# Kernel optimization log

Hardware: AMD Instinct MI355X
Metric: run time of the kernel (lower is better)

## Reference

```python
import jax, jax.numpy as jnp
import numpy as np

VX, VY = 0.2, 0.2
X_OFFSET = VX / 2 + 0.0      # pc_range[0] = 0
Y_OFFSET = VY / 2 + (-40.0)  # pc_range[1] = -40
BN_EPS = 1e-3
IN_CH, OUT_CH = 9, 64


def setup_inputs() -> dict:
    key = jax.random.key(0)
    k1, k2, k3, k4 = jax.random.split(key, 4)
    bs, V, P = 2, 12000, 100
    features = jax.random.normal(k1, (bs, V, P, 4), dtype=jnp.float32)
    num_points = jax.random.randint(k2, (bs, V), 0, 100, dtype=jnp.int32)
    coors = jax.random.randint(k3, (bs, V, 4), 0, 352, dtype=jnp.int32)
    W = jax.random.normal(k4, (IN_CH, OUT_CH), dtype=jnp.float32) * 0.1
    gamma = jnp.ones((OUT_CH,), dtype=jnp.float32)
    beta = jnp.zeros((OUT_CH,), dtype=jnp.float32)
    return {"features": features, "num_points": num_points, "coors": coors,
            "W": W, "gamma": gamma, "beta": beta}


def reference(features, num_points, coors, W, gamma, beta):
    bs, V, P, _ = features.shape
    dt = features.dtype
    npf = num_points.astype(dt)

    # cluster features: offset from per-pillar mean of xyz
    points_mean = features[..., :3].sum(axis=2, keepdims=True) / jnp.maximum(npf, 1.0)[:, :, None, None]
    f_cluster = features[..., :3] - points_mean

    # center features: offset from pillar center (coors[...,2] = x idx, coors[...,1] = y idx)
    coors_f = coors.astype(dt)
    fcx = features[..., 0] - (coors_f[:, :, 2][:, :, None] * VX + X_OFFSET)
    fcy = features[..., 1] - (coors_f[:, :, 1][:, :, None] * VY + Y_OFFSET)
    f_center = jnp.stack([fcx, fcy], axis=-1)

    feats = jnp.concatenate([features, f_cluster, f_center], axis=-1)  # [bs,V,P,9]

    # padding mask over points in each pillar
    mask = (num_points[:, :, None] > jnp.arange(P)).astype(dt)[..., None]
    feats = feats * mask

    # PFNLayer (last layer): Linear(no bias) -> BatchNorm1d(train-mode stats) -> ReLU -> max over points
    x = jnp.einsum('bvpi,io->bvpo', feats, W)  # [bs,V,P,64]
    mean = x.mean(axis=(0, 1, 2))
    var = x.var(axis=(0, 1, 2))  # biased variance, as torch BN uses for normalization
    x = (x - mean) * jax.lax.rsqrt(var + BN_EPS) * gamma + beta
    x = jax.nn.relu(x)
    return x.max(axis=2)  # [bs,V,64]
```

## Files before the change

### kernel.cpp

```cpp
#include <hip/hip_runtime.h>
#include <math.h>

#define NP 100
#define NPILLAR 24000
#define OUT_CH 64
#define NTOTAL 2400000.0
#define VXc 0.2f
#define VYc 0.2f
#define XOFF 0.1f
#define YOFF (-39.9f)
#define BN_EPS 1e-3
#define SB 1024

typedef __attribute__((ext_vector_type(8))) short bf16x8;
typedef __attribute__((ext_vector_type(16))) float f32x16;
typedef __attribute__((ext_vector_type(4))) unsigned int uint4v;

__device__ __forceinline__ unsigned int f2bf(float x) {
    unsigned int b = __builtin_bit_cast(unsigned int, x);
    b += 0x7FFFu + ((b >> 16) & 1u);
    return b >> 16;
}

__device__ __forceinline__ void build_f(const float4 p, float mx, float my, float mz,
                                        float cx, float cy, float* f) {
    f[0] = p.x; f[1] = p.y; f[2] = p.z; f[3] = p.w;
    f[4] = p.x - mx; f[5] = p.y - my; f[6] = p.z - mz;
    f[7] = p.x - cx; f[8] = p.y - cy;
}

__global__ __launch_bounds__(256) void pfn_stats(
    const float4* __restrict__ feat, const int* __restrict__ npts,
    const int* __restrict__ coors, float* __restrict__ part)
{
    const int tid = threadIdx.x;
    const int lane = tid & 63;
    const int wv = tid >> 6;
    const int gw = blockIdx.x * 4 + wv;
    const int nw = SB * 4;

    float s[54];
#pragma unroll
    for (int i = 0; i < 54; ++i) s[i] = 0.f;

    for (int pv = gw; pv < NPILLAR; pv += nw) {
        const float4* fp = feat + (size_t)pv * NP;
        float4 p0 = fp[lane];
        float4 p1 = (lane + 64 < NP) ? fp[lane + 64] : make_float4(0.f, 0.f, 0.f, 0.f);

        float sx = p0.x + p1.x, sy = p0.y + p1.y, sz = p0.z + p1.z;
#pragma unroll
        for (int off = 32; off; off >>= 1) {
            sx += __shfl_xor(sx, off);
            sy += __shfl_xor(sy, off);
            sz += __shfl_xor(sz, off);
        }
        int np_ = npts[pv];
        if (np_ > NP) np_ = NP;
        float inv = 1.f / fmaxf((float)np_, 1.f);
        float mx = sx * inv, my = sy * inv, mz = sz * inv;
        float cx = (float)coors[pv * 4 + 2] * VXc + XOFF;
        float cy = (float)coors[pv * 4 + 1] * VYc + YOFF;

        float f[9];
        if (lane < np_) {
            build_f(p0, mx, my, mz, cx, cy, f);
            int k = 9;
#pragma unroll
            for (int i = 0; i < 9; ++i) {
                s[i] += f[i];
#pragma unroll
                for (int j = i; j < 9; ++j) s[k++] = fmaf(f[i], f[j], s[k]);
            }
        }
        if (lane + 64 < np_) {
            build_f(p1, mx, my, mz, cx, cy, f);
            int k = 9;
#pragma unroll
            for (int i = 0; i < 9; ++i) {
                s[i] += f[i];
#pragma unroll
                for (int j = i; j < 9; ++j) s[k++] = fmaf(f[i], f[j], s[k]);
            }
        }
    }

#pragma unroll
    for (int i = 0; i < 54; ++i) {
#pragma unroll
        for (int off = 32; off; off >>= 1) s[i] += __shfl_xor(s[i], off);
    }

    __shared__ float red[4][54];
    if (lane == 0) {
#pragma unroll
        for (int i = 0; i < 54; ++i) red[wv][i] = s[i];
    }
    __syncthreads();
    if (tid < 64) {
        float v = 0.f;
        if (tid < 54)
            v = red[0][tid] + red[1][tid] + red[2][tid] + red[3][tid];
        part[blockIdx.x * 64 + tid] = v;
    }
}

__global__ __launch_bounds__(1024) void pfn_finalize(
    const float* __restrict__ part, const float* __restrict__ W,
    const float* __restrict__ gamma, const float* __restrict__ beta,
    float* __restrict__ scsh)
{
    __shared__ double red[16][64];
    __shared__ double dm[64];
    const int t = threadIdx.x;
    const int m = t & 63;
    const int chunk = t >> 6;

    double s = 0.0;
#pragma unroll 8
    for (int b = chunk * 64; b < chunk * 64 + 64; ++b)
        s += (double)part[b * 64 + m];
    red[chunk][m] = s;
    __syncthreads();
    if (t < 64) {
        double tot = 0.0;
#pragma unroll
        for (int c = 0; c < 16; ++c) tot += red[c][t];
        dm[t] = tot;
    }
    __syncthreads();
    if (t < 64) {
        double w[9];
#pragma unroll
        for (int i = 0; i < 9; ++i) w[i] = (double)W[i * OUT_CH + t];
        double mean = 0.0;
#pragma unroll
        for (int i = 0; i < 9; ++i) mean += dm[i] * w[i];
        mean /= NTOTAL;
        double ex2 = 0.0;
        int k = 9;
#pragma unroll
        for (int i = 0; i < 9; ++i) {
#pragma unroll
            for (int j = i; j < 9; ++j) {
                double c = dm[k++];
                ex2 += (i == j ? 1.0 : 2.0) * c * w[i] * w[j];
            }
        }
        ex2 /= NTOTAL;
        double var = ex2 - mean * mean;
        double scale = (double)gamma[t] / sqrt(var + BN_EPS);
        double shift = (double)beta[t] - mean * scale;
        scsh[t] = (float)scale;
        scsh[OUT_CH + t] = (float)shift;
    }
}

__global__ __launch_bounds__(256) void pfn_out(
    const float4* __restrict__ feat, const int* __restrict__ npts,
    const int* __restrict__ coors, const float* __restrict__ W,
    const float* __restrict__ scsh, float* __restrict__ out)
{
    const int tid = threadIdx.x;
    const int lane = tid & 63;
    const int wv = tid >> 6;
    const int pv = blockIdx.x * 4 + wv;

    const int col = lane & 31;
    const int kbase = (lane >> 5) * 8;
    bf16x8 bfr0, bfr1;
#pragma unroll
    for (int i = 0; i < 8; ++i) {
        int k = kbase + i;
        float w0 = (k < 9) ? W[k * OUT_CH + col] : 0.f;
        float w1 = (k < 9) ? W[k * OUT_CH + 32 + col] : 0.f;
        bfr0[i] = (short)f2bf(w0);
        bfr1[i] = (short)f2bf(w1);
    }

    const float4* fp = feat + (size_t)pv * NP;
    float4 p0 = fp[lane];
    float4 p1 = (lane + 64 < NP) ? fp[lane + 64] : make_float4(0.f, 0.f, 0.f, 0.f);

    float sx = p0.x + p1.x, sy = p0.y + p1.y, sz = p0.z + p1.z;
#pragma unroll
    for (int off = 32; off; off >>= 1) {
        sx += __shfl_xor(sx, off);
        sy += __shfl_xor(sy, off);
        sz += __shfl_xor(sz, off);
    }
    int np_ = npts[pv];
    if (np_ > NP) np_ = NP;
    float inv = 1.f / fmaxf((float)np_, 1.f);
    float mx = sx * inv, my = sy * inv, mz = sz * inv;
    float cx = (float)coors[pv * 4 + 2] * VXc + XOFF;
    float cy = (float)coors[pv * 4 + 1] * VYc + YOFF;

    unsigned int A[5], B[5];
    {
        float f[9];
        if (lane < np_) {
            build_f(p0, mx, my, mz, cx, cy, f);
            A[0] = f2bf(f[0]) | (f2bf(f[1]) << 16);
            A[1] = f2bf(f[2]) | (f2bf(f[3]) << 16);
            A[2] = f2bf(f[4]) | (f2bf(f[5]) << 16);
            A[3] = f2bf(f[6]) | (f2bf(f[7]) << 16);
            A[4] = f2bf(f[8]);
        } else {
#pragma unroll
            for (int i = 0; i < 5; ++i) A[i] = 0u;
        }
        if (lane + 64 < np_) {
            build_f(p1, mx, my, mz, cx, cy, f);
            B[0] = f2bf(f[0]) | (f2bf(f[1]) << 16);
            B[1] = f2bf(f[2]) | (f2bf(f[3]) << 16);
            B[2] = f2bf(f[4]) | (f2bf(f[5]) << 16);
            B[3] = f2bf(f[6]) | (f2bf(f[7]) << 16);
            B[4] = f2bf(f[8]);
        } else {
#pragma unroll
            for (int i = 0; i < 5; ++i) B[i] = 0u;
        }
    }

    f32x16 cz;
#pragma unroll
    for (int i = 0; i < 16; ++i) cz[i] = 0.f;

    float xmx0 = -INFINITY, xmx1 = -INFINITY;
    float xmn0 = INFINITY, xmn1 = INFINITY;
    const bool lo = (lane < 32);
    const int nmt = (np_ + 31) >> 5;

    for (int mt = 0; mt < nmt; ++mt) {
        const int src = ((mt & 1) << 5) + col;
        unsigned int w0, w1, w2, w3, w4;
        if (mt < 2) {
            w0 = __shfl((int)A[0], src); w1 = __shfl((int)A[1], src);
            w2 = __shfl((int)A[2], src); w3 = __shfl((int)A[3], src);
            w4 = __shfl((int)A[4], src);
        } else {
            w0 = __shfl((int)B[0], src); w1 = __shfl((int)B[1], src);
            w2 = __shfl((int)B[2], src); w3 = __shfl((int)B[3], src);
            w4 = __shfl((int)B[4], src);
        }
        uint4v av = {lo ? w0 : w4, lo ? w1 : 0u, lo ? w2 : 0u, lo ? w3 : 0u};
        bf16x8 afr = __builtin_bit_cast(bf16x8, av);

        f32x16 c0 = __builtin_amdgcn_mfma_f32_32x32x16_bf16(afr, bfr0, cz, 0, 0, 0);
        f32x16 c1 = __builtin_amdgcn_mfma_f32_32x32x16_bf16(afr, bfr1, cz, 0, 0, 0);
#pragma unroll
        for (int r = 0; r < 16; r += 2) {
            xmx0 = fmaxf(xmx0, fmaxf(c0[r], c0[r + 1]));
            xmn0 = fminf(xmn0, fminf(c0[r], c0[r + 1]));
            xmx1 = fmaxf(xmx1, fmaxf(c1[r], c1[r + 1]));
            xmn1 = fminf(xmn1, fminf(c1[r], c1[r + 1]));
        }
    }

    if (np_ < NP) {
        xmx0 = fmaxf(xmx0, 0.f); xmx1 = fmaxf(xmx1, 0.f);
        xmn0 = fminf(xmn0, 0.f); xmn1 = fminf(xmn1, 0.f);
    }

    xmx0 = fmaxf(xmx0, __shfl_xor(xmx0, 32));
    xmx1 = fmaxf(xmx1, __shfl_xor(xmx1, 32));
    xmn0 = fminf(xmn0, __shfl_xor(xmn0, 32));
    xmn1 = fminf(xmn1, __shfl_xor(xmn1, 32));

    float xmx = lo ? xmx0 : xmx1;
    float xmn = lo ? xmn0 : xmn1;
    float scale = scsh[lane];
    float shift = scsh[OUT_CH + lane];
    out[(size_t)pv * OUT_CH + lane] =
        fmaxf(fmaf(scale, (scale >= 0.f) ? xmx : xmn, shift), 0.f);
}

extern "C" void kernel_launch(void* const* d_in, const int* in_sizes, int n_in,
                              void* d_out, int out_size, void* d_ws, size_t ws_size,
                              hipStream_t stream) {
    const float4* feat = (const float4*)d_in[0];
    const int* npts    = (const int*)d_in[1];
    const int* coors   = (const int*)d_in[2];
    const float* W     = (const float*)d_in[3];
    const float* gamma = (const float*)d_in[4];
    const float* beta  = (const float*)d_in[5];

    float* part = (float*)d_ws;
    float* scsh = part + SB * 64;

    pfn_stats<<<SB, 256, 0, stream>>>(feat, npts, coors, part);
    pfn_finalize<<<1, 1024, 0, stream>>>(part, W, gamma, beta, scsh);
    pfn_out<<<NPILLAR / 4, 256, 0, stream>>>(feat, npts, coors, W, scsh,
                                             (float*)d_out);
}
```

Before: 53.53 us.

## Fuse stats and matmul into one pass over features, apply BN in second kernel

Merges the statistics pass and the MFMA projection/max pass so the 38 MB feature tensor is read once instead of twice. Per-pillar raw max and min of the projected values go to workspace, and a new apply kernel computes BN scale/shift from the partial moments and applies them elementwise. This drops one kernel launch and one full feature read, at the cost of writing and reading two 6 MB max/min buffers and redundantly recomputing the finalize reduction in every apply block. It also clamps max/min against zero unconditionally for every pillar.

```diff
diff --git a/kernel.cpp b/kernel.cpp
--- a/kernel.cpp
+++ b/kernel.cpp
@@ -10,7 +10,9 @@
 #define XOFF 0.1f
 #define YOFF (-39.9f)
 #define BN_EPS 1e-3
-#define SB 1024
+#define G1 1024
+#define NWAVE1 (G1 * 4)
+#define G2 256
 
 typedef __attribute__((ext_vector_type(8))) short bf16x8;
 typedef __attribute__((ext_vector_type(16))) float f32x16;
@@ -29,21 +31,48 @@
     f[7] = p.x - cx; f[8] = p.y - cy;
 }
 
-__global__ __launch_bounds__(256) void pfn_stats(
+__device__ __forceinline__ void moments(float* s, const float* f) {
+    int k = 9;
+#pragma unroll
+    for (int i = 0; i < 9; ++i) {
+        s[i] += f[i];
+#pragma unroll
+        for (int j = i; j < 9; ++j) { s[k] = fmaf(f[i], f[j], s[k]); ++k; }
+    }
+}
+
+__global__ __launch_bounds__(256, 3) void pfn_main(
     const float4* __restrict__ feat, const int* __restrict__ npts,
-    const int* __restrict__ coors, float* __restrict__ part)
+    const int* __restrict__ coors, const float* __restrict__ W,
+    float* __restrict__ xmax_ws, float* __restrict__ xmin_ws,
+    float* __restrict__ part)
 {
     const int tid = threadIdx.x;
     const int lane = tid & 63;
     const int wv = tid >> 6;
     const int gw = blockIdx.x * 4 + wv;
-    const int nw = SB * 4;
+
+    const int col = lane & 31;
+    const int kbase = (lane >> 5) * 8;
+    const bool lo = (lane < 32);
+    bf16x8 bfr0, bfr1;
+#pragma unroll
+    for (int i = 0; i < 8; ++i) {
+        int k = kbase + i;
+        float w0 = (k < 9) ? W[k * OUT_CH + col] : 0.f;
+        float w1 = (k < 9) ? W[k * OUT_CH + 32 + col] : 0.f;
+        bfr0[i] = (short)f2bf(w0);
+        bfr1[i] = (short)f2bf(w1);
+    }
+    f32x16 cz;
+#pragma unroll
+    for (int i = 0; i < 16; ++i) cz[i] = 0.f;
 
     float s[54];
 #pragma unroll
     for (int i = 0; i < 54; ++i) s[i] = 0.f;
 
-    for (int pv = gw; pv < NPILLAR; pv += nw) {
+    for (int pv = gw; pv < NPILLAR; pv += NWAVE1) {
         const float4* fp = feat + (size_t)pv * NP;
         float4 p0 = fp[lane];
         float4 p1 = (lane + 64 < NP) ? fp[lane + 64] : make_float4(0.f, 0.f, 0.f, 0.f);
@@ -62,27 +91,78 @@
         float cx = (float)coors[pv * 4 + 2] * VXc + XOFF;
         float cy = (float)coors[pv * 4 + 1] * VYc + YOFF;
 
-        float f[9];
-        if (lane < np_) {
-            build_f(p0, mx, my, mz, cx, cy, f);
-            int k = 9;
-#pragma unroll
-            for (int i = 0; i < 9; ++i) {
-                s[i] += f[i];
-#pragma unroll
-                for (int j = i; j < 9; ++j) s[k++] = fmaf(f[i], f[j], s[k]);
-            }
-        }
-        if (lane + 64 < np_) {
-            build_f(p1, mx, my, mz, cx, cy, f);
-            int k = 9;
-#pragma unroll
-            for (int i = 0; i < 9; ++i) {
-                s[i] += f[i];
-#pragma unroll
-                for (int j = i; j < 9; ++j) s[k++] = fmaf(f[i], f[j], s[k]);
-            }
-        }
+        unsigned int A[5], B[5];
+        {
+            float f[9];
+            if (lane < np_) {
+                build_f(p0, mx, my, mz, cx, cy, f);
+                moments(s, f);
+                A[0] = f2bf(f[0]) | (f2bf(f[1]) << 16);
+                A[1] = f2bf(f[2]) | (f2bf(f[3]) << 16);
+                A[2] = f2bf(f[4]) | (f2bf(f[5]) << 16);
+                A[3] = f2bf(f[6]) | (f2bf(f[7]) << 16);
+                A[4] = f2bf(f[8]);
+            } else {
+#pragma unroll
+                for (int i = 0; i < 5; ++i) A[i] = 0u;
+            }
+            if (lane + 64 < np_) {
+                build_f(p1, mx, my, mz, cx, cy, f);
+                moments(s, f);
+                B[0] = f2bf(f[0]) | (f2bf(f[1]) << 16);
+                B[1] = f2bf(f[2]) | (f2bf(f[3]) << 16);
+                B[2] = f2bf(f[4]) | (f2bf(f[5]) << 16);
+                B[3] = f2bf(f[6]) | (f2bf(f[7]) << 16);
+                B[4] = f2bf(f[8]);
+            } else {
+#pragma unroll
+                for (int i = 0; i < 5; ++i) B[i] = 0u;
+            }
+        }
+
+        float xmx0 = -INFINITY, xmx1 = -INFINITY;
+        float xmn0 = INFINITY, xmn1 = INFINITY;
+        const int nmt = (np_ + 31) >> 5;
+
+        for (int mt = 0; mt < nmt; ++mt) {
+            const int src = ((mt & 1) << 5) + col;
+            unsigned int w0, w1, w2, w3, w4;
+            if (mt < 2) {
+                w0 = __shfl((int)A[0], src); w1 = __shfl((int)A[1], src);
+                w2 = __shfl((int)A[2], src); w3 = __shfl((int)A[3], src);
+                w4 = __shfl((int)A[4], src);
+            } else {
+                w0 = __shfl((int)B[0], src); w1 = __shfl((int)B[1], src);
+                w2 = __shfl((int)B[2], src); w3 = __shfl((int)B[3], src);
+                w4 = __shfl((int)B[4], src);
+            }
+            uint4v av = {lo ? w0 : w4, lo ? w1 : 0u, lo ? w2 : 0u, lo ? w3 : 0u};
+            bf16x8 afr = __builtin_bit_cast(bf16x8, av);
+
+            f32x16 c0 = __builtin_amdgcn_mfma_f32_32x32x16_bf16(afr, bfr0, cz, 0, 0, 0);
+#pragma unroll
+            for (int r = 0; r < 16; r += 2) {
+                xmx0 = fmaxf(xmx0, fmaxf(c0[r], c0[r + 1]));
+                xmn0 = fminf(xmn0, fminf(c0[r], c0[r + 1]));
+            }
+            f32x16 c1 = __builtin_amdgcn_mfma_f32_32x32x16_bf16(afr, bfr1, cz, 0, 0, 0);
+#pragma unroll
+            for (int r = 0; r < 16; r += 2) {
+                xmx1 = fmaxf(xmx1, fmaxf(c1[r], c1[r + 1]));
+                xmn1 = fminf(xmn1, fminf(c1[r], c1[r + 1]));
+            }
+        }
+
+        xmx0 = fmaxf(xmx0, 0.f); xmx1 = fmaxf(xmx1, 0.f);
+        xmn0 = fminf(xmn0, 0.f); xmn1 = fminf(xmn1, 0.f);
+
+        xmx0 = fmaxf(xmx0, __shfl_xor(xmx0, 32));
+        xmx1 = fmaxf(xmx1, __shfl_xor(xmx1, 32));
+        xmn0 = fminf(xmn0, __shfl_xor(xmn0, 32));
+        xmn1 = fminf(xmn1, __shfl_xor(xmn1, 32));
+
+        xmax_ws[(size_t)pv * OUT_CH + lane] = lo ? xmx0 : xmx1;
+        xmin_ws[(size_t)pv * OUT_CH + lane] = lo ? xmn0 : xmn1;
     }
 
 #pragma unroll
@@ -90,7 +170,6 @@
 #pragma unroll
         for (int off = 32; off; off >>= 1) s[i] += __shfl_xor(s[i], off);
     }
-
     __shared__ float red[4][54];
     if (lane == 0) {
 #pragma unroll
@@ -101,34 +180,35 @@
         float v = 0.f;
         if (tid < 54)
             v = red[0][tid] + red[1][tid] + red[2][tid] + red[3][tid];
-        part[blockIdx.x * 64 + tid] = v;
-    }
-}
-
-__global__ __launch_bounds__(1024) void pfn_finalize(
+        part[(size_t)blockIdx.x * 64 + tid] = v;
+    }
+}
+
+__global__ __launch_bounds__(256) void pfn_apply(
     const float* __restrict__ part, const float* __restrict__ W,
     const float* __restrict__ gamma, const float* __restrict__ beta,
-    float* __restrict__ scsh)
+    const float4* __restrict__ xmax_ws, const float4* __restrict__ xmin_ws,
+    float4* __restrict__ out)
 {
-    __shared__ double red[16][64];
+    __shared__ double dred[4][64];
     __shared__ double dm[64];
+    __shared__ float sc_s[64], sh_s[64];
+
     const int t = threadIdx.x;
     const int m = t & 63;
-    const int chunk = t >> 6;
+    const int g = t >> 6;
 
     double s = 0.0;
-#pragma unroll 8
-    for (int b = chunk * 64; b < chunk * 64 + 64; ++b)
-        s += (double)part[b * 64 + m];
-    red[chunk][m] = s;
-    __syncthreads();
+    for (int b = g; b < G1; b += 4)
+        s += (double)part[(size_t)b * 64 + m];
+    dred[g][m] = s;
+    __syncthreads();
+
     if (t < 64) {
-        double tot = 0.0;
-#pragma unroll
-        for (int c = 0; c < 16; ++c) tot += red[c][t];
-        dm[t] = tot;
-    }
-    __syncthreads();
+        dm[t] = dred[0][t] + dred[1][t] + dred[2][t] + dred[3][t];
+    }
+    __syncthreads();
+
     if (t < 64) {
         double w[9];
 #pragma unroll
@@ -143,137 +223,43 @@
         for (int i = 0; i < 9; ++i) {
 #pragma unroll
             for (int j = i; j < 9; ++j) {
-                double c = dm[k++];
-                ex2 += (i == j ? 1.0 : 2.0) * c * w[i] * w[j];
+                ex2 += (i == j ? 1.0 : 2.0) * dm[k] * w[i] * w[j];
+                ++k;
             }
         }
         ex2 /= NTOTAL;
         double var = ex2 - mean * mean;
         double scale = (double)gamma[t] / sqrt(var + BN_EPS);
         double shift = (double)beta[t] - mean * scale;
-        scsh[t] = (float)scale;
-        scsh[OUT_CH + t] = (float)shift;
-    }
-}
-
-__global__ __launch_bounds__(256) void pfn_out(
-    const float4* __restrict__ feat, const int* __restrict__ npts,
-    const int* __restrict__ coors, const float* __restrict__ W,
-    const float* __restrict__ scsh, float* __restrict__ out)
-{
-    const int tid = threadIdx.x;
-    const int lane = tid & 63;
-    const int wv = tid >> 6;
-    const int pv = blockIdx.x * 4 + wv;
-
-    const int col = lane & 31;
-    const int kbase = (lane >> 5) * 8;
-    bf16x8 bfr0, bfr1;
-#pragma unroll
-    for (int i = 0; i < 8; ++i) {
-        int k = kbase + i;
-        float w0 = (k < 9) ? W[k * OUT_CH + col] : 0.f;
-        float w1 = (k < 9) ? W[k * OUT_CH + 32 + col] : 0.f;
-        bfr0[i] = (short)f2bf(w0);
-        bfr1[i] = (short)f2bf(w1);
-    }
-
-    const float4* fp = feat + (size_t)pv * NP;
-    float4 p0 = fp[lane];
-    float4 p1 = (lane + 64 < NP) ? fp[lane + 64] : make_float4(0.f, 0.f, 0.f, 0.f);
-
-    float sx = p0.x + p1.x, sy = p0.y + p1.y, sz = p0.z + p1.z;
-#pragma unroll
-    for (int off = 32; off; off >>= 1) {
-        sx += __shfl_xor(sx, off);
-        sy += __shfl_xor(sy, off);
-        sz += __shfl_xor(sz, off);
-    }
-    int np_ = npts[pv];
-    if (np_ > NP) np_ = NP;
-    float inv = 1.f / fmaxf((float)np_, 1.f);
-    float mx = sx * inv, my = sy * inv, mz = sz * inv;
-    float cx = (float)coors[pv * 4 + 2] * VXc + XOFF;
-    float cy = (float)coors[pv * 4 + 1] * VYc + YOFF;
-
-    unsigned int A[5], B[5];
-    {
-        float f[9];
-        if (lane < np_) {
-            build_f(p0, mx, my, mz, cx, cy, f);
-            A[0] = f2bf(f[0]) | (f2bf(f[1]) << 16);
-            A[1] = f2bf(f[2]) | (f2bf(f[3]) << 16);
-            A[2] = f2bf(f[4]) | (f2bf(f[5]) << 16);
-            A[3] = f2bf(f[6]) | (f2bf(f[7]) << 16);
-            A[4] = f2bf(f[8]);
-        } else {
-#pragma unroll
-            for (int i = 0; i < 5; ++i) A[i] = 0u;
-        }
-        if (lane + 64 < np_) {
-            build_f(p1, mx, my, mz, cx, cy, f);
-            B[0] = f2bf(f[0]) | (f2bf(f[1]) << 16);
-            B[1] = f2bf(f[2]) | (f2bf(f[3]) << 16);
-            B[2] = f2bf(f[4]) | (f2bf(f[5]) << 16);
-            B[3] = f2bf(f[6]) | (f2bf(f[7]) << 16);
-            B[4] = f2bf(f[8]);
-        } else {
-#pragma unroll
-            for (int i = 0; i < 5; ++i) B[i] = 0u;
-        }
-    }
-
-    f32x16 cz;
-#pragma unroll
-    for (int i = 0; i < 16; ++i) cz[i] = 0.f;
-
-    float xmx0 = -INFINITY, xmx1 = -INFINITY;
-    float xmn0 = INFINITY, xmn1 = INFINITY;
-    const bool lo = (lane < 32);
-    const int nmt = (np_ + 31) >> 5;
-
-    for (int mt = 0; mt < nmt; ++mt) {
-        const int src = ((mt & 1) << 5) + col;
-        unsigned int w0, w1, w2, w3, w4;
-        if (mt < 2) {
-            w0 = __shfl((int)A[0], src); w1 = __shfl((int)A[1], src);
-            w2 = __shfl((int)A[2], src); w3 = __shfl((int)A[3], src);
-            w4 = __shfl((int)A[4], src);
-        } else {
-            w0 = __shfl((int)B[0], src); w1 = __shfl((int)B[1], src);
-            w2 = __shfl((int)B[2], src); w3 = __shfl((int)B[3], src);
-            w4 = __shfl((int)B[4], src);
-        }
-        uint4v av = {lo ? w0 : w4, lo ? w1 : 0u, lo ? w2 : 0u, lo ? w3 : 0u};
-        bf16x8 afr = __builtin_bit_cast(bf16x8, av);
-
-        f32x16 c0 = __builtin_amdgcn_mfma_f32_32x32x16_bf16(afr, bfr0, cz, 0, 0, 0);
-        f32x16 c1 = __builtin_amdgcn_mfma_f32_32x32x16_bf16(afr, bfr1, cz, 0, 0, 0);
-#pragma unroll
-        for (int r = 0; r < 16; r += 2) {
-            xmx0 = fmaxf(xmx0, fmaxf(c0[r], c0[r + 1]));
-            xmn0 = fminf(xmn0, fminf(c0[r], c0[r + 1]));
-            xmx1 = fmaxf(xmx1, fmaxf(c1[r], c1[r + 1]));
-            xmn1 = fminf(xmn1, fminf(c1[r], c1[r + 1]));
-        }
-    }
-
-    if (np_ < NP) {
-        xmx0 = fmaxf(xmx0, 0.f); xmx1 = fmaxf(xmx1, 0.f);
-        xmn0 = fminf(xmn0, 0.f); xmn1 = fminf(xmn1, 0.f);
-    }
-
-    xmx0 = fmaxf(xmx0, __shfl_xor(xmx0, 32));
-    xmx1 = fmaxf(xmx1, __shfl_xor(xmx1, 32));
-    xmn0 = fminf(xmn0, __shfl_xor(xmn0, 32));
-    xmn1 = fminf(xmn1, __shfl_xor(xmn1, 32));
-
-    float xmx = lo ? xmx0 : xmx1;
-    float xmn = lo ? xmn0 : xmn1;
-    float scale = scsh[lane];
-    float shift = scsh[OUT_CH + lane];
-    out[(size_t)pv * OUT_CH + lane] =
-        fmaxf(fmaf(scale, (scale >= 0.f) ? xmx : xmn, shift), 0.f);
+        sc_s[t] = (float)scale;
+        sh_s[t] = (float)shift;
+    }
+    __syncthreads();
+
+    const int N4 = NPILLAR * OUT_CH / 4;
+    for (int i = blockIdx.x * 256 + t; i < N4; i += G2 * 256) {
+        float4 mx = xmax_ws[i];
+        float4 mn = xmin_ws[i];
+        int c = (i & 15) * 4;
+        float4 r;
+        {
+            float sc = sc_s[c + 0], sh = sh_s[c + 0];
+            r.x = fmaxf(fmaf(sc, (sc >= 0.f) ? mx.x : mn.x, sh), 0.f);
+        }
+        {
+            float sc = sc_s[c + 1], sh = sh_s[c + 1];
+            r.y = fmaxf(fmaf(sc, (sc >= 0.f) ? mx.y : mn.y, sh), 0.f);
+        }
+        {
+            float sc = sc_s[c + 2], sh = sh_s[c + 2];
+            r.z = fmaxf(fmaf(sc, (sc >= 0.f) ? mx.z : mn.z, sh), 0.f);
+        }
+        {
+            float sc = sc_s[c + 3], sh = sh_s[c + 3];
+            r.w = fmaxf(fmaf(sc, (sc >= 0.f) ? mx.w : mn.w, sh), 0.f);
+        }
+        out[i] = r;
+    }
 }
 
 extern "C" void kernel_launch(void* const* d_in, const int* in_sizes, int n_in,
@@ -286,11 +272,12 @@
     const float* gamma = (const float*)d_in[4];
     const float* beta  = (const float*)d_in[5];
 
-    float* part = (float*)d_ws;
-    float* scsh = part + SB * 64;
-
-    pfn_stats<<<SB, 256, 0, stream>>>(feat, npts, coors, part);
-    pfn_finalize<<<1, 1024, 0, stream>>>(part, W, gamma, beta, scsh);
-    pfn_out<<<NPILLAR / 4, 256, 0, stream>>>(feat, npts, coors, W, scsh,
-                                             (float*)d_out);
-}
+    float* xmax_ws = (float*)d_ws;
+    float* xmin_ws = xmax_ws + (size_t)NPILLAR * OUT_CH;
+    float* part    = xmin_ws + (size_t)NPILLAR * OUT_CH;
+
+    pfn_main<<<G1, 256, 0, stream>>>(feat, npts, coors, W, xmax_ws, xmin_ws, part);
+    pfn_apply<<<G2, 256, 0, stream>>>(part, W, gamma, beta,
+                                      (const float4*)xmax_ws, (const float4*)xmin_ws,
+                                      (float4*)d_out);
+}
```

Result: slower. 106.9 us (+99.7%).
